# Optimization experiments

Measured on AMD Instinct MI355X. Metric: run time of the kernel, lower is better.

## Reference

```python
import jax, jax.numpy as jnp
import numpy as np

N = 524288
H = 128
EPS = 1e-4
SYMP_N = 32  # min(N, 32)
# loss weights from init_kwargs
W_RECON, W_CONS, W_EVO, W_SYMP, W_GAUGE = 1.0, 10.0, 5.0, 0.1, 5.0


def _mlp(x, W1, b1, W2, b2, W3, b3):
    h = jnp.tanh(x @ W1 + b1)
    h = jnp.tanh(h @ W2 + b2)
    return h @ W3 + b3


def _encode(p, q, params):
    out = _mlp(jnp.stack([p, q], axis=-1), *params)  # [N,2]
    return out[:, 0], out[:, 1]


def _decode(P, Q, params):
    out = _mlp(jnp.stack([P, Q], axis=-1), *params)
    return out[:, 0], out[:, 1]


def setup_inputs() -> dict:
    key = jax.random.key(0)
    ks = jax.random.split(key, 24)
    f32 = jnp.float32

    def nrm(k, shape, scale=1.0):
        return (scale * jax.random.normal(k, shape, dtype=f32))

    inp = {
        'p0': nrm(ks[0], (N,)),
        'q0': nrm(ks[1], (N,)),
        'p1': nrm(ks[2], (N,)),
        'q1': nrm(ks[3], (N,)),
        'omega_values': jax.random.uniform(ks[4], (N,), dtype=f32, minval=0.5, maxval=2.0),
        'dt': jnp.asarray(0.05, dtype=f32),
        'P_true': nrm(ks[5], (N,)),
        'Q_true': nrm(ks[6], (N,)),
        # encoder params (2 -> H -> H -> 2), fan-in scaled init
        'enc_W1': nrm(ks[7], (2, H), 1.0 / np.sqrt(2.0)),
        'enc_b1': jnp.zeros((H,), f32),
        'enc_W2': nrm(ks[8], (H, H), 1.0 / np.sqrt(H)),
        'enc_b2': jnp.zeros((H,), f32),
        'enc_W3': nrm(ks[9], (H, 2), 1.0 / np.sqrt(H)),
        'enc_b3': jnp.zeros((2,), f32),
        # decoder params
        'dec_W1': nrm(ks[10], (2, H), 1.0 / np.sqrt(2.0)),
        'dec_b1': jnp.zeros((H,), f32),
        'dec_W2': nrm(ks[11], (H, H), 1.0 / np.sqrt(H)),
        'dec_b2': jnp.zeros((H,), f32),
        'dec_W3': nrm(ks[12], (H, 2), 1.0 / np.sqrt(H)),
        'dec_b3': jnp.zeros((2,), f32),
    }
    return inp


def _loss(p0, q0, p1, q1, omega_values, dt, P_true, Q_true, enc, dec):
    P0, Q0 = _encode(p0, q0, enc)
    P1, Q1 = _encode(p1, q1, enc)
    p0_recon, q0_recon = _decode(P0, Q0, dec)

    recon_loss = jnp.mean((p0 - p0_recon) ** 2 + (q0 - q0_recon) ** 2)
    conservation_loss = jnp.mean((P0 - P1) ** 2)
    evolution_loss = jnp.mean(1.0 - jnp.cos((Q1 - Q0) - omega_values * dt))

    # symplectic loss: batched central finite differences over first 32 samples
    pi, qi = p0[:SYMP_N], q0[:SYMP_N]
    pp = jnp.concatenate([pi + EPS, pi - EPS, pi, pi])          # [4*32]
    qq = jnp.concatenate([qi, qi, qi + EPS, qi - EPS])
    P, Q = _encode(pp, qq, enc)
    P_pp, P_pm, P_qp, P_qm = jnp.split(P, 4)
    Q_pp, Q_pm, Q_qp, Q_qm = jnp.split(Q, 4)
    inv2e = 1.0 / (2.0 * EPS)
    dP_dp = (P_pp - P_pm) * inv2e
    dP_dq = (P_qp - P_qm) * inv2e
    dQ_dp = (Q_pp - Q_pm) * inv2e
    dQ_dq = (Q_qp - Q_qm) * inv2e
    pb = dP_dq * dQ_dp - dP_dp * dQ_dq
    symplectic_loss = jnp.mean((jnp.abs(pb) - 1.0) ** 2)

    gauge_loss = jnp.mean((P0 - P_true) ** 2) + jnp.mean(1.0 - jnp.cos(Q0 - Q_true))

    total = (W_RECON * recon_loss + W_CONS * conservation_loss
             + W_EVO * evolution_loss + W_SYMP * symplectic_loss
             + W_GAUGE * gauge_loss)
    return jnp.stack([total, recon_loss, conservation_loss,
                      evolution_loss, symplectic_loss, gauge_loss])


def reference(p0, q0, p1, q1, omega_values, dt, P_true, Q_true,
              enc_W1, enc_b1, enc_W2, enc_b2, enc_W3, enc_b3,
              dec_W1, dec_b1, dec_W2, dec_b2, dec_W3, dec_b3):
    enc = (enc_W1, enc_b1, enc_W2, enc_b2, enc_W3, enc_b3)
    dec = (dec_W1, dec_b1, dec_W2, dec_b2, dec_W3, dec_b3)
    return _loss(p0, q0, p1, q1, omega_values, dt, P_true, Q_true, enc, dec)
```

## Files before the change

kernel.cpp:

```cpp
#include <hip/hip_runtime.h>
#include <stdint.h>
#include <math.h>


constexpr float EPS_FD = 1e-4f;
constexpr float K2LOG2E = 2.8853900817779268f;
constexpr int NBLK = 256;

typedef float f32x4 __attribute__((ext_vector_type(4)));
typedef short s16x8 __attribute__((ext_vector_type(8)));

__device__ __forceinline__ float tanh_pre(float x) {
  float e = __builtin_amdgcn_exp2f(x);
  return 1.0f - 2.0f * __builtin_amdgcn_rcpf(e + 1.0f);
}
__device__ __forceinline__ float cos_fast(float x) {
  return __builtin_amdgcn_cosf(x * 0.15915494309189535f);
}
__device__ __forceinline__ unsigned bf16rne(float f) {
  union { float f; unsigned u; } v; v.f = f;
  return (v.u + 0x7FFFu + ((v.u >> 16) & 1u)) >> 16;
}
__device__ __forceinline__ unsigned pack2rne(float a, float b) {
  return bf16rne(a) | (bf16rne(b) << 16);
}
__device__ __forceinline__ unsigned packbf(float lo, float hi) {
  union { float f; unsigned u; } a, b; a.f = lo; b.f = hi;
  return __builtin_amdgcn_perm(b.u + 0x8000u, a.u + 0x8000u, 0x07060302u);
}

template<bool SCAT>
__device__ __forceinline__ void layer1_frags(
    float pe, float qe, unsigned* hrow,
    float w100, float w101, float w110, float w111, float b10, float b11,
    int lane, int quad, int l15, s16x8 (&A)[4])
{
#pragma unroll
  for (int ee = 0; ee < 16; ee++) {
    int src = SCAT ? (16 * (ee >> 2) + (ee & 3)) : ee;
    float p = __shfl(pe, src, 64);
    float q = __shfl(qe, src, 64);
    float a0 = tanh_pre(fmaf(p, w100, fmaf(q, w110, b10)));
    float a1 = tanh_pre(fmaf(p, w101, fmaf(q, w111, b11)));
    hrow[ee * 68 + lane] = packbf(a0, a1);
  }
  __builtin_amdgcn_wave_barrier();
#pragma unroll
  for (int s = 0; s < 4; s++) {
    uint4 u = *reinterpret_cast<const uint4*>(&hrow[l15 * 68 + 16 * s + 4 * quad]);
    A[s] = *reinterpret_cast<s16x8*>(&u);
  }
  __builtin_amdgcn_wave_barrier();
}

__device__ __forceinline__ void enc_pair(
    float p0e, float q0e, float p1e, float q1e,
    unsigned* hrow, const uint4* Bf, const float* epi,
    float w100, float w101, float w110, float w111, float b10, float b11,
    int lane, int quad, int l15,
    float& P0v, float& Q0v, float& P1v, float& Q1v)
{
  s16x8 A0[4], A1[4];
  layer1_frags<false>(p0e, q0e, hrow, w100, w101, w110, w111, b10, b11,
                      lane, quad, l15, A0);
  layer1_frags<false>(p1e, q1e, hrow, w100, w101, w110, w111, b10, b11,
                      lane, quad, l15, A1);

  float sP0[4] = {0,0,0,0}, sQ0[4] = {0,0,0,0};
  float sP1[4] = {0,0,0,0}, sQ1[4] = {0,0,0,0};
#pragma unroll
  for (int t = 0; t < 8; t++) {
    float b2v = epi[16 * t + l15];
    f32x4 acc0 = {b2v, b2v, b2v, b2v};
    f32x4 acc1 = {b2v, b2v, b2v, b2v};
#pragma unroll
    for (int s = 0; s < 4; s++) {
      uint4 bu = Bf[(s * 8 + t) * 64 + lane];
      s16x8 Bv = *reinterpret_cast<s16x8*>(&bu);
      acc0 = __builtin_amdgcn_mfma_f32_16x16x32_bf16(A0[s], Bv, acc0, 0, 0, 0);
      acc1 = __builtin_amdgcn_mfma_f32_16x16x32_bf16(A1[s], Bv, acc1, 0, 0, 0);
    }
    float w3Pv = epi[128 + 16 * t + l15];
    float w3Qv = epi[256 + 16 * t + l15];
#pragma unroll
    for (int r = 0; r < 4; r++) {
      float h0 = tanh_pre(acc0[r]);
      float h1 = tanh_pre(acc1[r]);
      sP0[r] = fmaf(h0, w3Pv, sP0[r]); sQ0[r] = fmaf(h0, w3Qv, sQ0[r]);
      sP1[r] = fmaf(h1, w3Pv, sP1[r]); sQ1[r] = fmaf(h1, w3Qv, sQ1[r]);
    }
  }
#pragma unroll
  for (int m = 1; m < 16; m <<= 1) {
#pragma unroll
    for (int r = 0; r < 4; r++) {
      sP0[r] += __shfl_xor(sP0[r], m, 64);
      sQ0[r] += __shfl_xor(sQ0[r], m, 64);
      sP1[r] += __shfl_xor(sP1[r], m, 64);
      sQ1[r] += __shfl_xor(sQ1[r], m, 64);
    }
  }
  P0v = (l15 == 0) ? sP0[0] : (l15 == 1) ? sP0[1] : (l15 == 2) ? sP0[2] : sP0[3];
  Q0v = (l15 == 0) ? sQ0[0] : (l15 == 1) ? sQ0[1] : (l15 == 2) ? sQ0[2] : sQ0[3];
  P1v = (l15 == 0) ? sP1[0] : (l15 == 1) ? sP1[1] : (l15 == 2) ? sP1[2] : sP1[3];
  Q1v = (l15 == 0) ? sQ1[0] : (l15 == 1) ? sQ1[1] : (l15 == 2) ? sQ1[2] : sQ1[3];
}

__device__ __forceinline__ void dec_pass(
    float pe, float qe, unsigned* hrow, const uint4* Bf, const float* epi,
    float w100, float w101, float w110, float w111, float b10, float b11,
    int lane, int quad, int l15, float& vP, float& vQ)
{
  s16x8 A[4];
  layer1_frags<true>(pe, qe, hrow, w100, w101, w110, w111, b10, b11,
                     lane, quad, l15, A);
  float sP[4] = {0,0,0,0}, sQ[4] = {0,0,0,0};
#pragma unroll
  for (int t = 0; t < 8; t++) {
    float b2v = epi[16 * t + l15];
    f32x4 acc = {b2v, b2v, b2v, b2v};
#pragma unroll
    for (int s = 0; s < 4; s++) {
      uint4 bu = Bf[(s * 8 + t) * 64 + lane];
      s16x8 Bv = *reinterpret_cast<s16x8*>(&bu);
      acc = __builtin_amdgcn_mfma_f32_16x16x32_bf16(A[s], Bv, acc, 0, 0, 0);
    }
    float w3Pv = epi[128 + 16 * t + l15];
    float w3Qv = epi[256 + 16 * t + l15];
#pragma unroll
    for (int r = 0; r < 4; r++) {
      float h = tanh_pre(acc[r]);
      sP[r] = fmaf(h, w3Pv, sP[r]);
      sQ[r] = fmaf(h, w3Qv, sQ[r]);
    }
  }
#pragma unroll
  for (int m = 1; m < 16; m <<= 1) {
#pragma unroll
    for (int r = 0; r < 4; r++) {
      sP[r] += __shfl_xor(sP[r], m, 64);
      sQ[r] += __shfl_xor(sQ[r], m, 64);
    }
  }
  vP = (l15 == 0) ? sP[0] : (l15 == 1) ? sP[1] : (l15 == 2) ? sP[2] : sP[3];
  vQ = (l15 == 0) ? sQ[0] : (l15 == 1) ? sQ[1] : (l15 == 2) ? sQ[2] : sQ[3];
}

__global__ __launch_bounds__(1024, 1) void mlp_main(
    const float* __restrict__ p0, const float* __restrict__ q0,
    const float* __restrict__ p1, const float* __restrict__ q1,
    const float* __restrict__ eW1, const float* __restrict__ eb1,
    const float* __restrict__ eW2, const float* __restrict__ eb2,
    const float* __restrict__ eW3, const float* __restrict__ eb3,
    const float* __restrict__ dW1, const float* __restrict__ db1,
    const float* __restrict__ dW2, const float* __restrict__ db2,
    const float* __restrict__ dW3, const float* __restrict__ db3,
    const float* __restrict__ omega, const float* __restrict__ Pt,
    const float* __restrict__ Qt, const float* __restrict__ dtp,
    float* __restrict__ acc5, unsigned* __restrict__ counter,
    float* __restrict__ PQ, float* __restrict__ out, int n)
{
  __shared__ uint4 BfE[2048];
  __shared__ uint4 BfD[2048];
  __shared__ unsigned h1s[16][16 * 68 + 4];
  __shared__ float encEpi[384];
  __shared__ float decEpi[384];
  __shared__ float red[16][5];
  __shared__ unsigned lastflag;

  int tid = threadIdx.x;
#pragma unroll
  for (int it = 0; it < 8; it++) {
    int id = tid + it * 1024;
    int jj = id & 3, ln = (id >> 2) & 63, f = id >> 8;
    int s = f >> 3, t = f & 7;
    int k   = 32 * s + 8 * (ln >> 4) + 2 * jj;
    int col = 16 * t + (ln & 15);
    ((unsigned*)BfE)[id] = pack2rne(eW2[k * 128 + col] * K2LOG2E,
                                    eW2[(k + 1) * 128 + col] * K2LOG2E);
    ((unsigned*)BfD)[id] = pack2rne(dW2[k * 128 + col] * K2LOG2E,
                                    dW2[(k + 1) * 128 + col] * K2LOG2E);
  }
  if (tid < 128) {
    encEpi[tid]       = eb2[tid] * K2LOG2E;
    encEpi[128 + tid] = eW3[2 * tid];
    encEpi[256 + tid] = eW3[2 * tid + 1];
  } else if (tid < 256) {
    int u = tid - 128;
    decEpi[u]       = db2[u] * K2LOG2E;
    decEpi[128 + u] = dW3[2 * u];
    decEpi[256 + u] = dW3[2 * u + 1];
  }

  int wave = tid >> 6, lane = tid & 63;
  int quad = lane >> 4, l15 = lane & 15;

  float ew100 = eW1[2 * lane] * K2LOG2E,       ew101 = eW1[2 * lane + 1] * K2LOG2E;
  float ew110 = eW1[128 + 2 * lane] * K2LOG2E, ew111 = eW1[128 + 2 * lane + 1] * K2LOG2E;
  float eb10 = eb1[2 * lane] * K2LOG2E, eb11 = eb1[2 * lane + 1] * K2LOG2E;
  float dw100 = dW1[2 * lane] * K2LOG2E,       dw101 = dW1[2 * lane + 1] * K2LOG2E;
  float dw110 = dW1[128 + 2 * lane] * K2LOG2E, dw111 = dW1[128 + 2 * lane + 1] * K2LOG2E;
  float db10 = db1[2 * lane] * K2LOG2E, db11 = db1[2 * lane + 1] * K2LOG2E;
  float eb3P = eb3[0], eb3Q = eb3[1];
  float db3P = db3[0], db3Q = db3[1];
  float dt = dtp[0];
  float s0 = 0.f, s1 = 0.f, s2 = 0.f, s3 = 0.f, s4 = 0.f;
  __syncthreads();

  int nwaves = gridDim.x * 16;
  int gwave  = blockIdx.x * 16 + wave;
  int ntiles = (n + 15) >> 4;
  unsigned* hrow = &h1s[wave][0];

  if (gwave < 128) {
    int r = gwave;
    int m = r & 31, c = r >> 5;
    float p = p0[m], q = q0[m];
    p += (c == 0) ? EPS_FD : (c == 1) ? -EPS_FD : 0.f;
    q += (c == 2) ? EPS_FD : (c == 3) ? -EPS_FD : 0.f;
    float* hf = (float*)hrow;
    int t0 = 2 * lane, t1 = 2 * lane + 1;
    float h0 = tanhf(fmaf(p, eW1[t0], fmaf(q, eW1[128 + t0], eb1[t0])));
    float h1v = tanhf(fmaf(p, eW1[t1], fmaf(q, eW1[128 + t1], eb1[t1])));
    hf[t0] = h0; hf[t1] = h1v;
    __builtin_amdgcn_wave_barrier();
    float a0 = eb2[t0], a1 = eb2[t1];
#pragma unroll 8
    for (int k = 0; k < 128; k++) {
      float hk = hf[k];
      a0 = fmaf(hk, eW2[k * 128 + t0], a0);
      a1 = fmaf(hk, eW2[k * 128 + t1], a1);
    }
    float g0 = tanhf(a0), g1 = tanhf(a1);
    float cP = fmaf(g0, eW3[2 * t0],     g1 * eW3[2 * t1]);
    float cQ = fmaf(g0, eW3[2 * t0 + 1], g1 * eW3[2 * t1 + 1]);
#pragma unroll
    for (int mm = 1; mm < 64; mm <<= 1) {
      cP += __shfl_xor(cP, mm, 64);
      cQ += __shfl_xor(cQ, mm, 64);
    }
    if (lane == 0) {
      atomicExch(&PQ[2 * r],     cP + eb3P);
      atomicExch(&PQ[2 * r + 1], cQ + eb3Q);
    }
    __builtin_amdgcn_wave_barrier();
  }

  for (int tile = gwave; tile < ntiles; tile += nwaves) {
    int base = tile * 16;
    int e = base + l15; if (e >= n) e = n - 1;
    float p0e = p0[e], q0e = q0[e];
    float p1e = p1[e], q1e = q1[e];
    int o = base + quad * 4 + l15;
    int o16 = base + quad * 4 + (l15 & 3);
    if (o16 >= n) o16 = n - 1;
    float Lom = omega[o16], LPt = Pt[o16], LQt = Qt[o16];
    float Lp0 = p0[o16],    Lq0 = q0[o16];

    float P0v, Q0v, P1v, Q1v, RPv, RQv;
    enc_pair(p0e, q0e, p1e, q1e, hrow, BfE, encEpi,
             ew100, ew101, ew110, ew111, eb10, eb11,
             lane, quad, l15, P0v, Q0v, P1v, Q1v);
    P0v += eb3P; Q0v += eb3Q;
    P1v += eb3P; Q1v += eb3Q;
    dec_pass(P0v, Q0v, hrow, BfD, decEpi,
             dw100, dw101, dw110, dw111, db10, db11,
             lane, quad, l15, RPv, RQv);
    RPv += db3P; RQv += db3Q;

    if (l15 < 4 && o < n) {
      float dp = Lp0 - RPv, dq = Lq0 - RQv;
      s0 += dp * dp + dq * dq;
      float d1 = P0v - P1v; s1 += d1 * d1;
      s2 += 1.0f - cos_fast(Q1v - Q0v - Lom * dt);
      float g = P0v - LPt; s3 += g * g;
      s4 += 1.0f - cos_fast(Q0v - LQt);
    }
  }

#pragma unroll
  for (int m = 1; m < 64; m <<= 1) {
    s0 += __shfl_xor(s0, m, 64);
    s1 += __shfl_xor(s1, m, 64);
    s2 += __shfl_xor(s2, m, 64);
    s3 += __shfl_xor(s3, m, 64);
    s4 += __shfl_xor(s4, m, 64);
  }
  if (lane == 0) {
    red[wave][0] = s0; red[wave][1] = s1; red[wave][2] = s2;
    red[wave][3] = s3; red[wave][4] = s4;
  }
  __syncthreads();
  if (tid == 0) {
#pragma unroll
    for (int i = 0; i < 5; i++) {
      float v = 0.f;
#pragma unroll
      for (int w = 0; w < 16; w++) v += red[w][i];
      atomicAdd(&acc5[i], v);
    }
    __threadfence();
    unsigned prev = atomicAdd(counter, 1u);
    lastflag = (prev == gridDim.x - 1) ? 1u : 0u;
  }
  __syncthreads();
  if (lastflag) {
    __threadfence();
    if (tid < 64) {
      float v = 0.f;
      if (tid < 32) {
        float Ppp = atomicAdd(&PQ[2 * tid], 0.f);
        float Qpp = atomicAdd(&PQ[2 * tid + 1], 0.f);
        float Ppm = atomicAdd(&PQ[2 * (32 + tid)], 0.f);
        float Qpm = atomicAdd(&PQ[2 * (32 + tid) + 1], 0.f);
        float Pqp = atomicAdd(&PQ[2 * (64 + tid)], 0.f);
        float Qqp = atomicAdd(&PQ[2 * (64 + tid) + 1], 0.f);
        float Pqm = atomicAdd(&PQ[2 * (96 + tid)], 0.f);
        float Qqm = atomicAdd(&PQ[2 * (96 + tid) + 1], 0.f);
        float inv2e = 1.0f / (2.0f * EPS_FD);
        float dPdp = (Ppp - Ppm) * inv2e, dPdq = (Pqp - Pqm) * inv2e;
        float dQdp = (Qpp - Qpm) * inv2e, dQdq = (Qqp - Qqm) * inv2e;
        float pb = dPdq * dQdp - dPdp * dQdq;
        float d = fabsf(pb) - 1.0f;
        v = d * d;
      }
#pragma unroll
      for (int m = 1; m < 64; m <<= 1) v += __shfl_xor(v, m, 64);
      if (tid == 0) {
        float inv_n = 1.0f / (float)n;
        float recon = atomicAdd(&acc5[0], 0.f) * inv_n;
        float cons  = atomicAdd(&acc5[1], 0.f) * inv_n;
        float evo   = atomicAdd(&acc5[2], 0.f) * inv_n;
        float gauge = (atomicAdd(&acc5[3], 0.f) + atomicAdd(&acc5[4], 0.f)) * inv_n;
        float symp  = v * (1.0f / 32.0f);
        float total = recon + 10.0f * cons + 5.0f * evo + 0.1f * symp + 5.0f * gauge;
        out[0] = total; out[1] = recon; out[2] = cons;
        out[3] = evo;   out[4] = symp;  out[5] = gauge;
      }
    }
  }
}

extern "C" void kernel_launch(void* const* d_in, const int* in_sizes, int n_in,
                              void* d_out, int out_size, void* d_ws, size_t ws_size,
                              hipStream_t stream)
{
  const float* p0    = (const float*)d_in[0];
  const float* q0    = (const float*)d_in[1];
  const float* p1    = (const float*)d_in[2];
  const float* q1    = (const float*)d_in[3];
  const float* omega = (const float*)d_in[4];
  const float* dtp   = (const float*)d_in[5];
  const float* Pt    = (const float*)d_in[6];
  const float* Qt    = (const float*)d_in[7];
  const float* encW1 = (const float*)d_in[8];
  const float* encb1 = (const float*)d_in[9];
  const float* encW2 = (const float*)d_in[10];
  const float* encb2 = (const float*)d_in[11];
  const float* encW3 = (const float*)d_in[12];
  const float* encb3 = (const float*)d_in[13];
  const float* decW1 = (const float*)d_in[14];
  const float* decb1 = (const float*)d_in[15];
  const float* decW2 = (const float*)d_in[16];
  const float* decb2 = (const float*)d_in[17];
  const float* decW3 = (const float*)d_in[18];
  const float* decb3 = (const float*)d_in[19];

  int n = in_sizes[0];
  float* acc5 = (float*)d_ws;
  unsigned* counter = (unsigned*)(acc5 + 8);
  float* PQ = (float*)(acc5 + 16);

  hipMemsetAsync(acc5, 0, 64, stream);

  mlp_main<<<NBLK, 1024, 0, stream>>>(
      p0, q0, p1, q1,
      encW1, encb1, encW2, encb2, encW3, encb3,
      decW1, decb1, decW2, decb2, decW3, decb3,
      omega, Pt, Qt, dtp, acc5, counter, PQ, (float*)d_out, n);
}
```

Before: 269.1 us.

## Move decoder weight fragments to global via prep kernel, halve LDS, double blocks

```diff
diff --git a/kernel.cpp b/kernel.cpp
--- a/kernel.cpp
+++ b/kernel.cpp
@@ -5,7 +5,7 @@
 
 constexpr float EPS_FD = 1e-4f;
 constexpr float K2LOG2E = 2.8853900817779268f;
-constexpr int NBLK = 256;
+constexpr int NBLK = 512;
 
 typedef float f32x4 __attribute__((ext_vector_type(4)));
 typedef short s16x8 __attribute__((ext_vector_type(8)));
@@ -27,6 +27,20 @@
 __device__ __forceinline__ unsigned packbf(float lo, float hi) {
   union { float f; unsigned u; } a, b; a.f = lo; b.f = hi;
   return __builtin_amdgcn_perm(b.u + 0x8000u, a.u + 0x8000u, 0x07060302u);
+}
+
+__global__ __launch_bounds__(1024) void prep_dec(
+    const float* __restrict__ dW2, unsigned* __restrict__ frag,
+    float* __restrict__ acc5, unsigned* __restrict__ counter)
+{
+  int id = blockIdx.x * 1024 + threadIdx.x;
+  if (id < 6) { if (id < 5) acc5[id] = 0.f; else *counter = 0u; }
+  int jj = id & 3, ln = (id >> 2) & 63, f = id >> 8;
+  int s = f >> 3, t = f & 7;
+  int k   = 32 * s + 8 * (ln >> 4) + 2 * jj;
+  int col = 16 * t + (ln & 15);
+  frag[id] = pack2rne(dW2[k * 128 + col] * K2LOG2E,
+                      dW2[(k + 1) * 128 + col] * K2LOG2E);
 }
 
 template<bool SCAT>
@@ -35,22 +49,30 @@
     float w100, float w101, float w110, float w111, float b10, float b11,
     int lane, int quad, int l15, s16x8 (&A)[4])
 {
-#pragma unroll
-  for (int ee = 0; ee < 16; ee++) {
-    int src = SCAT ? (16 * (ee >> 2) + (ee & 3)) : ee;
-    float p = __shfl(pe, src, 64);
-    float q = __shfl(qe, src, 64);
-    float a0 = tanh_pre(fmaf(p, w100, fmaf(q, w110, b10)));
-    float a1 = tanh_pre(fmaf(p, w101, fmaf(q, w111, b11)));
-    hrow[ee * 68 + lane] = packbf(a0, a1);
-  }
-  __builtin_amdgcn_wave_barrier();
-#pragma unroll
-  for (int s = 0; s < 4; s++) {
-    uint4 u = *reinterpret_cast<const uint4*>(&hrow[l15 * 68 + 16 * s + 4 * quad]);
-    A[s] = *reinterpret_cast<s16x8*>(&u);
-  }
-  __builtin_amdgcn_wave_barrier();
+  int halfsel = l15 >> 3;
+  int rowid   = l15 & 7;
+#pragma unroll
+  for (int half = 0; half < 2; half++) {
+#pragma unroll
+    for (int ee = 0; ee < 8; ee++) {
+      int elem = half * 8 + ee;
+      int src = SCAT ? (16 * (elem >> 2) + (elem & 3)) : elem;
+      float p = __shfl(pe, src, 64);
+      float q = __shfl(qe, src, 64);
+      float a0 = tanh_pre(fmaf(p, w100, fmaf(q, w110, b10)));
+      float a1 = tanh_pre(fmaf(p, w101, fmaf(q, w111, b11)));
+      hrow[ee * 68 + lane] = packbf(a0, a1);
+    }
+    __builtin_amdgcn_wave_barrier();
+    if (halfsel == half) {
+#pragma unroll
+      for (int s = 0; s < 4; s++) {
+        uint4 u = *reinterpret_cast<const uint4*>(&hrow[rowid * 68 + 16 * s + 4 * quad]);
+        A[s] = *reinterpret_cast<s16x8*>(&u);
+      }
+    }
+    __builtin_amdgcn_wave_barrier();
+  }
 }
 
 __device__ __forceinline__ void enc_pair(
@@ -107,7 +129,8 @@
 }
 
 __device__ __forceinline__ void dec_pass(
-    float pe, float qe, unsigned* hrow, const uint4* Bf, const float* epi,
+    float pe, float qe, unsigned* hrow, const uint4* __restrict__ Bf,
+    const float* epi,
     float w100, float w101, float w110, float w111, float b10, float b11,
     int lane, int quad, int l15, float& vP, float& vQ)
 {
@@ -153,16 +176,16 @@
     const float* __restrict__ eW2, const float* __restrict__ eb2,
     const float* __restrict__ eW3, const float* __restrict__ eb3,
     const float* __restrict__ dW1, const float* __restrict__ db1,
-    const float* __restrict__ dW2, const float* __restrict__ db2,
+    const uint4* __restrict__ decFrag, const float* __restrict__ db2,
     const float* __restrict__ dW3, const float* __restrict__ db3,
+    const float* __restrict__ eW2raw,
     const float* __restrict__ omega, const float* __restrict__ Pt,
     const float* __restrict__ Qt, const float* __restrict__ dtp,
     float* __restrict__ acc5, unsigned* __restrict__ counter,
     float* __restrict__ PQ, float* __restrict__ out, int n)
 {
   __shared__ uint4 BfE[2048];
-  __shared__ uint4 BfD[2048];
-  __shared__ unsigned h1s[16][16 * 68 + 4];
+  __shared__ unsigned h1s[16][8 * 68 + 4];
   __shared__ float encEpi[384];
   __shared__ float decEpi[384];
   __shared__ float red[16][5];
@@ -178,8 +201,6 @@
     int col = 16 * t + (ln & 15);
     ((unsigned*)BfE)[id] = pack2rne(eW2[k * 128 + col] * K2LOG2E,
                                     eW2[(k + 1) * 128 + col] * K2LOG2E);
-    ((unsigned*)BfD)[id] = pack2rne(dW2[k * 128 + col] * K2LOG2E,
-                                    dW2[(k + 1) * 128 + col] * K2LOG2E);
   }
   if (tid < 128) {
     encEpi[tid]       = eb2[tid] * K2LOG2E;
@@ -228,8 +249,8 @@
 #pragma unroll 8
     for (int k = 0; k < 128; k++) {
       float hk = hf[k];
-      a0 = fmaf(hk, eW2[k * 128 + t0], a0);
-      a1 = fmaf(hk, eW2[k * 128 + t1], a1);
+      a0 = fmaf(hk, eW2raw[k * 128 + t0], a0);
+      a1 = fmaf(hk, eW2raw[k * 128 + t1], a1);
     }
     float g0 = tanhf(a0), g1 = tanhf(a1);
     float cP = fmaf(g0, eW3[2 * t0],     g1 * eW3[2 * t1]);
@@ -263,7 +284,7 @@
              lane, quad, l15, P0v, Q0v, P1v, Q1v);
     P0v += eb3P; Q0v += eb3Q;
     P1v += eb3P; Q1v += eb3Q;
-    dec_pass(P0v, Q0v, hrow, BfD, decEpi,
+    dec_pass(P0v, Q0v, hrow, decFrag, decEpi,
              dw100, dw101, dw110, dw111, db10, db11,
              lane, quad, l15, RPv, RQv);
     RPv += db3P; RQv += db3Q;
@@ -370,12 +391,14 @@
   float* acc5 = (float*)d_ws;
   unsigned* counter = (unsigned*)(acc5 + 8);
   float* PQ = (float*)(acc5 + 16);
-
-  hipMemsetAsync(acc5, 0, 64, stream);
+  unsigned* decFrag = (unsigned*)(acc5 + 512);
+
+  prep_dec<<<8, 1024, 0, stream>>>(decW2, decFrag, acc5, counter);
 
   mlp_main<<<NBLK, 1024, 0, stream>>>(
       p0, q0, p1, q1,
       encW1, encb1, encW2, encb2, encW3, encb3,
-      decW1, decb1, decW2, decb2, decW3, decb3,
+      decW1, decb1, (const uint4*)decFrag, decb2, decW3, decb3,
+      encW2,
       omega, Pt, Qt, dtp, acc5, counter, PQ, (float*)d_out, n);
 }
```

Result: slower. 372.3 us (+38.3%).
